# Performance work log

Hardware: AMD Instinct MI355X
Metric: run time of the kernel (lower is better)

## Reference

```python
import jax, jax.numpy as jnp
import numpy as np

B, S, E, F = 64, 8192, 8, 32  # batch, seq, embed_dim(=n_qubits), ffn_dim


def setup_inputs() -> dict:
    key = jax.random.key(0)
    k_x, k_t, k_w1, k_b1, k_w2, k_b2 = jax.random.split(key, 6)
    x = jax.random.normal(k_x, (B, S, E), dtype=jnp.float32)
    theta = jax.random.normal(k_t, (E,), dtype=jnp.float32)  # trainable RX angles
    lim1 = 1.0 / np.sqrt(E)
    lim2 = 1.0 / np.sqrt(F)
    w1 = jax.random.uniform(k_w1, (E, F), jnp.float32, -lim1, lim1)
    b1 = jax.random.uniform(k_b1, (F,), jnp.float32, -lim1, lim1)
    w2 = jax.random.uniform(k_w2, (F, E), jnp.float32, -lim2, lim2)
    b2 = jax.random.uniform(k_b2, (E,), jnp.float32, -lim2, lim2)
    return {"x": x, "theta": theta, "w1": w1, "b1": b1, "w2": w2, "b2": b2}


def reference(x, theta, w1, b1, w2, b2):
    # Quantum circuit: per wire i, RX(x_i) then RX(theta_i) on |0>, measure PauliZ.
    # Single-qubit RX gates compose: <Z> after RX(phi)|0> = cos(phi). Wires are
    # independent (no entangling gates), so MeasureAll(PauliZ) = cos(x + theta).
    q_out = jnp.cos(x + theta)                      # [B, S, E]
    h = jax.nn.relu(q_out @ w1 + b1)                # [B, S, F]
    return h @ w2 + b2                              # [B, S, E]
```

## Files before the change

### kernel.cpp

```cpp
#include <hip/hip_runtime.h>


#define TPB 256

__global__ __launch_bounds__(TPB, 8) void ffq_kernel(
    const float4* __restrict__ xv,
    const float*  __restrict__ theta,
    const float*  __restrict__ w1,
    const float*  __restrict__ b1,
    const float*  __restrict__ w2,
    const float*  __restrict__ b2,
    float4*       __restrict__ outv)
{
    const int g = blockIdx.x * TPB + threadIdx.x;

    float th[8], bb2[8];
#pragma unroll
    for (int e = 0; e < 8; ++e) { th[e] = theta[e]; bb2[e] = b2[e]; }

    const float4 a = xv[2 * g];
    const float4 c = xv[2 * g + 1];

    float q[8], o[8];
    q[0] = __cosf(a.x + th[0]);
    q[1] = __cosf(a.y + th[1]);
    q[2] = __cosf(a.z + th[2]);
    q[3] = __cosf(a.w + th[3]);
    q[4] = __cosf(c.x + th[4]);
    q[5] = __cosf(c.y + th[5]);
    q[6] = __cosf(c.z + th[6]);
    q[7] = __cosf(c.w + th[7]);
#pragma unroll
    for (int e = 0; e < 8; ++e) o[e] = bb2[e];

#pragma unroll 2
    for (int f = 0; f < 32; ++f) {
        const float bb = b1[f];
        float wa[8], wb[8];
#pragma unroll
        for (int e = 0; e < 8; ++e) wa[e] = w1[e * 32 + f];
#pragma unroll
        for (int e = 0; e < 8; ++e) wb[e] = w2[f * 8 + e];
        float h = bb;
#pragma unroll
        for (int e = 0; e < 8; ++e) h = fmaf(q[e], wa[e], h);
        h = fmaxf(h, 0.0f);
#pragma unroll
        for (int e = 0; e < 8; ++e) o[e] = fmaf(h, wb[e], o[e]);
    }

    outv[2 * g]     = make_float4(o[0], o[1], o[2], o[3]);
    outv[2 * g + 1] = make_float4(o[4], o[5], o[6], o[7]);
}

extern "C" void kernel_launch(void* const* d_in, const int* in_sizes, int n_in,
                              void* d_out, int out_size, void* d_ws, size_t ws_size,
                              hipStream_t stream) {
    const float* x     = (const float*)d_in[0];
    const float* theta = (const float*)d_in[1];
    const float* w1    = (const float*)d_in[2];
    const float* b1    = (const float*)d_in[3];
    const float* w2    = (const float*)d_in[4];
    const float* b2    = (const float*)d_in[5];
    float* out = (float*)d_out;

    const int ntok = in_sizes[0] / 8;
    const int grid = (ntok + TPB - 1) / TPB;

    ffq_kernel<<<grid, TPB, 0, stream>>>(
        (const float4*)x, theta, w1, b1, w2, b2, (float4*)out);
}
```

Measured before the change: 83.69 us.

## Compute the two-layer FFN with fp16 MFMA on 16-token tiles

Replaces the per-thread scalar FMA loops with two fp16 16x16x32 MFMA stages per 16-token tile, using ds_bpermute to reshuffle the hidden activations between the layers. The grid becomes persistent (1024 blocks) with a grid-stride loop over tiles and a one-tile prefetch of x. This aims to offload the dense arithmetic to matrix cores, but it lowers precision to fp16 and leaves only 16 lanes per wave doing loads and cosines.

```diff
diff --git a/kernel.cpp b/kernel.cpp
--- a/kernel.cpp
+++ b/kernel.cpp
@@ -3,54 +3,138 @@
 
 #define TPB 256
 
-__global__ __launch_bounds__(TPB, 8) void ffq_kernel(
+typedef _Float16 h8 __attribute__((ext_vector_type(8)));
+typedef __fp16   fp16x2 __attribute__((ext_vector_type(2)));
+typedef float    f4 __attribute__((ext_vector_type(4)));
+
+union H2I { fp16x2 h; int i; };
+union I4H8 { int i[4]; h8 h; };
+
+__device__ __forceinline__ int pack_f16(float a, float b) {
+    H2I u;
+    u.h = __builtin_amdgcn_cvt_pkrtz(a, b);
+    return u.i;
+}
+
+__global__ __launch_bounds__(TPB) void ffq_kernel(
     const float4* __restrict__ xv,
     const float*  __restrict__ theta,
     const float*  __restrict__ w1,
     const float*  __restrict__ b1,
     const float*  __restrict__ w2,
     const float*  __restrict__ b2,
-    float4*       __restrict__ outv)
+    float4*       __restrict__ outv,
+    int ntile, int nwaves)
 {
-    const int g = blockIdx.x * TPB + threadIdx.x;
+    const int tid  = threadIdx.x;
+    const int lane = tid & 63;
+    const int widx = tid >> 6;
+    const int quad = lane >> 4;
+    const int m16  = lane & 15;
 
-    float th[8], bb2[8];
+    h8 a1lo, a1hi, a2;
 #pragma unroll
-    for (int e = 0; e < 8; ++e) { th[e] = theta[e]; bb2[e] = b2[e]; }
+    for (int j = 0; j < 8; ++j) { a1lo[j] = (_Float16)0; a1hi[j] = (_Float16)0; a2[j] = (_Float16)0; }
 
-    const float4 a = xv[2 * g];
-    const float4 c = xv[2 * g + 1];
-
-    float q[8], o[8];
-    q[0] = __cosf(a.x + th[0]);
-    q[1] = __cosf(a.y + th[1]);
-    q[2] = __cosf(a.z + th[2]);
-    q[3] = __cosf(a.w + th[3]);
-    q[4] = __cosf(c.x + th[4]);
-    q[5] = __cosf(c.y + th[5]);
-    q[6] = __cosf(c.z + th[6]);
-    q[7] = __cosf(c.w + th[7]);
+    if (quad == 0) {
 #pragma unroll
-    for (int e = 0; e < 8; ++e) o[e] = bb2[e];
-
-#pragma unroll 2
-    for (int f = 0; f < 32; ++f) {
-        const float bb = b1[f];
-        float wa[8], wb[8];
+        for (int j = 0; j < 8; ++j) {
+            a1lo[j] = (_Float16)w1[j * 32 + m16];
+            a1hi[j] = (_Float16)w1[j * 32 + 16 + m16];
+        }
+    }
+    if (m16 < 8) {
 #pragma unroll
-        for (int e = 0; e < 8; ++e) wa[e] = w1[e * 32 + f];
-#pragma unroll
-        for (int e = 0; e < 8; ++e) wb[e] = w2[f * 8 + e];
-        float h = bb;
-#pragma unroll
-        for (int e = 0; e < 8; ++e) h = fmaf(q[e], wa[e], h);
-        h = fmaxf(h, 0.0f);
-#pragma unroll
-        for (int e = 0; e < 8; ++e) o[e] = fmaf(h, wb[e], o[e]);
+        for (int j = 0; j < 8; ++j)
+            a2[j] = (_Float16)w2[(quad * 8 + j) * 8 + m16];
     }
 
-    outv[2 * g]     = make_float4(o[0], o[1], o[2], o[3]);
-    outv[2 * g + 1] = make_float4(o[4], o[5], o[6], o[7]);
+    f4 c1lo0, c1hi0, c20;
+#pragma unroll
+    for (int r = 0; r < 4; ++r) {
+        c1lo0[r] = b1[quad * 4 + r];
+        c1hi0[r] = b1[16 + quad * 4 + r];
+        c20[r]   = (quad < 2) ? b2[quad * 4 + r] : 0.0f;
+    }
+
+    float th[8];
+#pragma unroll
+    for (int e = 0; e < 8; ++e) th[e] = theta[e];
+
+    const int addr0 = (((2 * quad) & 3) * 16 + m16) * 4;
+    const int addr1 = (((2 * quad + 1) & 3) * 16 + m16) * 4;
+
+    const int wid = blockIdx.x * (TPB / 64) + widx;
+
+    float4 curA = make_float4(0.f, 0.f, 0.f, 0.f);
+    float4 curC = curA;
+    if (wid < ntile && lane < 16) {
+        const int tok = wid * 16 + lane;
+        curA = xv[2 * tok];
+        curC = xv[2 * tok + 1];
+    }
+
+    for (int tile = wid; tile < ntile; tile += nwaves) {
+        float4 nA = curA, nC = curC;
+        const int nxt = tile + nwaves;
+        if (nxt < ntile && lane < 16) {
+            const int tok = nxt * 16 + lane;
+            nA = xv[2 * tok];
+            nC = xv[2 * tok + 1];
+        }
+
+        h8 bq;
+#pragma unroll
+        for (int j = 0; j < 8; ++j) bq[j] = (_Float16)0;
+        if (lane < 16) {
+            bq[0] = (_Float16)__cosf(curA.x + th[0]);
+            bq[1] = (_Float16)__cosf(curA.y + th[1]);
+            bq[2] = (_Float16)__cosf(curA.z + th[2]);
+            bq[3] = (_Float16)__cosf(curA.w + th[3]);
+            bq[4] = (_Float16)__cosf(curC.x + th[4]);
+            bq[5] = (_Float16)__cosf(curC.y + th[5]);
+            bq[6] = (_Float16)__cosf(curC.z + th[6]);
+            bq[7] = (_Float16)__cosf(curC.w + th[7]);
+        }
+
+        f4 c1lo = __builtin_amdgcn_mfma_f32_16x16x32_f16(a1lo, bq, c1lo0, 0, 0, 0);
+        f4 c1hi = __builtin_amdgcn_mfma_f32_16x16x32_f16(a1hi, bq, c1hi0, 0, 0, 0);
+
+#pragma unroll
+        for (int r = 0; r < 4; ++r) {
+            c1lo[r] = fmaxf(c1lo[r], 0.0f);
+            c1hi[r] = fmaxf(c1hi[r], 0.0f);
+        }
+
+        const int lo01 = pack_f16(c1lo[0], c1lo[1]);
+        const int lo23 = pack_f16(c1lo[2], c1lo[3]);
+        const int hi01 = pack_f16(c1hi[0], c1hi[1]);
+        const int hi23 = pack_f16(c1hi[2], c1hi[3]);
+
+        const int tL0 = __builtin_amdgcn_ds_bpermute(addr0, lo01);
+        const int tL1 = __builtin_amdgcn_ds_bpermute(addr0, lo23);
+        const int tL2 = __builtin_amdgcn_ds_bpermute(addr1, lo01);
+        const int tL3 = __builtin_amdgcn_ds_bpermute(addr1, lo23);
+        const int tH0 = __builtin_amdgcn_ds_bpermute(addr0, hi01);
+        const int tH1 = __builtin_amdgcn_ds_bpermute(addr0, hi23);
+        const int tH2 = __builtin_amdgcn_ds_bpermute(addr1, hi01);
+        const int tH3 = __builtin_amdgcn_ds_bpermute(addr1, hi23);
+
+        I4H8 bh;
+        bh.i[0] = (quad < 2) ? tL0 : tH0;
+        bh.i[1] = (quad < 2) ? tL1 : tH1;
+        bh.i[2] = (quad < 2) ? tL2 : tH2;
+        bh.i[3] = (quad < 2) ? tL3 : tH3;
+
+        f4 o = __builtin_amdgcn_mfma_f32_16x16x32_f16(a2, bh.h, c20, 0, 0, 0);
+
+        if (quad < 2) {
+            const int tok = tile * 16 + m16;
+            outv[2 * tok + quad] = make_float4(o[0], o[1], o[2], o[3]);
+        }
+
+        curA = nA; curC = nC;
+    }
 }
 
 extern "C" void kernel_launch(void* const* d_in, const int* in_sizes, int n_in,
@@ -64,9 +148,11 @@
     const float* b2    = (const float*)d_in[5];
     float* out = (float*)d_out;
 
-    const int ntok = in_sizes[0] / 8;
-    const int grid = (ntok + TPB - 1) / TPB;
+    const int ntok  = in_sizes[0] / 8;
+    const int ntile = ntok / 16;
+    const int grid  = 1024;
+    const int nwaves = grid * (TPB / 64);
 
     ffq_kernel<<<grid, TPB, 0, stream>>>(
-        (const float4*)x, theta, w1, b1, w2, b2, (float4*)out);
+        (const float4*)x, theta, w1, b1, w2, b2, (float4*)out, ntile, nwaves);
 }
```

Measured after the change: 81.27 us. 1.03x faster.
